# Optimization experiments

Measured on AMD Instinct MI355X. Metric: run time of the kernel, lower is better.

Reference implementation:

```python
import jax, jax.numpy as jnp
import numpy as np

B, S, HID = 2, 2048, 2048
NH, NKV, D = 32, 8, 64
G = NH // NKV  # kv groups


def rotate_half(x):
    x1, x2 = jnp.split(x, 2, axis=-1)
    return jnp.concatenate([-x2, x1], axis=-1)


def setup_inputs() -> dict:
    key = jax.random.key(0)
    ks = jax.random.split(key, 6)
    hidden_states = jax.random.normal(ks[0], (B, S, HID), dtype=jnp.float32)
    # rotary tables [S, D]
    inv_freq = 1.0 / (10000.0 ** (jnp.arange(0, D, 2, dtype=jnp.float32) / D))
    t = jnp.arange(S, dtype=jnp.float32)
    freqs = jnp.einsum('s,d->sd', t, inv_freq)
    emb = jnp.concatenate([freqs, freqs], axis=-1)
    cos, sin = jnp.cos(emb), jnp.sin(emb)
    # additive causal mask [B,1,S,S]
    causal = jnp.triu(jnp.full((S, S), -1e9, dtype=jnp.float32), k=1)
    attention_mask = jnp.broadcast_to(causal, (B, 1, S, S))
    sc = 0.02
    wq = jax.random.normal(ks[1], (HID, 2 * NH * D), dtype=jnp.float32) * sc
    wk = jax.random.normal(ks[2], (HID, NKV * D), dtype=jnp.float32) * sc
    wv = jax.random.normal(ks[3], (HID, NKV * D), dtype=jnp.float32) * sc
    wo = jax.random.normal(ks[4], (HID, HID), dtype=jnp.float32) * sc
    return {"hidden_states": hidden_states, "cos": cos, "sin": sin,
            "attention_mask": attention_mask, "wq": wq, "wk": wk, "wv": wv, "wo": wo}


def reference(hidden_states, cos, sin, attention_mask, wq, wk, wv, wo):
    b, s, _ = hidden_states.shape
    qg = hidden_states @ wq                      # [B,S,2*NH*D]
    q, gate = jnp.split(qg, 2, axis=-1)
    q = q.reshape(b, s, NH, D).transpose(0, 2, 1, 3)        # [B,NH,S,D]
    k = (hidden_states @ wk).reshape(b, s, NKV, D).transpose(0, 2, 1, 3)
    v = (hidden_states @ wv).reshape(b, s, NKV, D).transpose(0, 2, 1, 3)  # computed, unused (as in source)
    # RoPE (cos/sin broadcast over batch and heads)
    c = cos[None, None]; sn = sin[None, None]
    q = q * c + rotate_half(q) * sn
    k = k * c + rotate_half(k) * sn
    # GQA repeat_kv
    k = jnp.repeat(k, G, axis=1)                 # [B,NH,S,D]
    # no 1/sqrt(d) scaling in source
    attn = jnp.einsum('bhqd,bhkd->bhqk', q, k) + attention_mask
    w = jax.nn.softmax(attn.astype(jnp.float32), axis=-1).astype(q.dtype)
    # NOTE: source multiplies weights by key_states (not value_states) — reproduced faithfully
    out = jnp.einsum('bhqk,bhkd->bhqd', w, k)
    out = out.transpose(0, 2, 1, 3).reshape(b, s, HID)
    out = out * jax.nn.sigmoid(gate)
    return out @ wo
```

## Files before the change

### kernel.cpp

```cpp
#include <hip/hip_runtime.h>

typedef float f32x4 __attribute__((ext_vector_type(4)));
typedef short bf16x8 __attribute__((ext_vector_type(8)));

__device__ __forceinline__ float bf2f(unsigned short h) {
  return __uint_as_float(((unsigned int)h) << 16);
}
__device__ __forceinline__ unsigned short f2bf(float f) {
  unsigned int u = __float_as_uint(f);
  unsigned int r = u + 0x7fffu + ((u >> 16) & 1u);
  return (unsigned short)(r >> 16);
}
__device__ __forceinline__ float fast_exp2(float x) {
  return __builtin_amdgcn_exp2f(x);
}

__device__ __forceinline__ void gload_lds16(const void* g, void* l) {
  __builtin_amdgcn_global_load_lds((const __attribute__((address_space(1))) void*)g,
                                   (__attribute__((address_space(3))) void*)l, 16, 0, 0);
}

__global__ void conv_bf16(const float* __restrict__ src, unsigned short* __restrict__ dst, int n4) {
  for (int i = blockIdx.x * blockDim.x + threadIdx.x; i < n4; i += gridDim.x * blockDim.x) {
    float4 v = ((const float4*)src)[i];
    ushort4 o;
    o.x = f2bf(v.x); o.y = f2bf(v.y); o.z = f2bf(v.z); o.w = f2bf(v.w);
    ((ushort4*)dst)[i] = o;
  }
}

__global__ void tconv(const float* __restrict__ src, unsigned short* __restrict__ dst,
                      int C, int dstRowOff, int dstLD) {
  __shared__ float tile[32][33];
  int c0 = blockIdx.x * 32, r0 = blockIdx.y * 32;
  int tx = threadIdx.x, ty = threadIdx.y;
#pragma unroll
  for (int i = 0; i < 4; ++i)
    tile[ty + i * 8][tx] = src[(size_t)(r0 + ty + i * 8) * C + c0 + tx];
  __syncthreads();
#pragma unroll
  for (int i = 0; i < 4; ++i)
    dst[(size_t)(dstRowOff + c0 + ty + i * 8) * dstLD + r0 + tx] = f2bf(tile[tx][ty + i * 8]);
}

template <typename OutT>
__global__ __launch_bounds__(256) void gemm_bt(const unsigned short* __restrict__ A,
                                               const unsigned short* __restrict__ BT,
                                               OutT* __restrict__ C, int M, int N, int K) {
  __shared__ unsigned short As[128 * 64];
  __shared__ unsigned short Bs[128 * 64];
  const int tid = threadIdx.x;
  const int lane = tid & 63;
  const int wid = tid >> 6;
  const int g = lane >> 4, l15 = lane & 15;
  const int wr = wid >> 1, wc = wid & 1;
  const int bm = blockIdx.y, bn = blockIdx.x;
  const unsigned short* Ab = A + (size_t)bm * 128 * K;
  const unsigned short* Bb = BT + (size_t)bn * 128 * K;
  f32x4 acc[4][4] = {};
  int Rj[4], csj[4];
#pragma unroll
  for (int j = 0; j < 4; ++j) {
    int c = j * 256 + tid;
    Rj[j] = c >> 3;
    csj[j] = ((c & 7) ^ (Rj[j] & 7)) * 8;
  }
  for (int k0 = 0; k0 < K; k0 += 64) {
#pragma unroll
    for (int j = 0; j < 4; ++j) {
      gload_lds16(Ab + (size_t)Rj[j] * K + k0 + csj[j], &As[(j * 256 + (wid << 6)) * 8]);
      gload_lds16(Bb + (size_t)Rj[j] * K + k0 + csj[j], &Bs[(j * 256 + (wid << 6)) * 8]);
    }
    __syncthreads();
    bf16x8 af[4][2], bfr[4][2];
#pragma unroll
    for (int i = 0; i < 4; ++i)
#pragma unroll
      for (int kk = 0; kk < 2; ++kk) {
        int rowa = wr * 64 + i * 16 + l15;
        int cha = ((kk * 4 + g) ^ (rowa & 7)) * 8;
        af[i][kk] = *(const bf16x8*)&As[rowa * 64 + cha];
        int rowb = wc * 64 + i * 16 + l15;
        int chb = ((kk * 4 + g) ^ (rowb & 7)) * 8;
        bfr[i][kk] = *(const bf16x8*)&Bs[rowb * 64 + chb];
      }
    __builtin_amdgcn_s_setprio(1);
#pragma unroll
    for (int kk = 0; kk < 2; ++kk)
#pragma unroll
      for (int i = 0; i < 4; ++i)
#pragma unroll
        for (int j = 0; j < 4; ++j)
          acc[i][j] = __builtin_amdgcn_mfma_f32_16x16x32_bf16(af[i][kk], bfr[j][kk], acc[i][j], 0, 0, 0);
    __builtin_amdgcn_s_setprio(0);
    __syncthreads();
  }
  const int rbase = bm * 128 + wr * 64 + ((lane >> 4) << 2);
  const int cbase = bn * 128 + wc * 64 + l15;
#pragma unroll
  for (int i = 0; i < 4; ++i)
#pragma unroll
    for (int j = 0; j < 4; ++j)
#pragma unroll
      for (int r = 0; r < 4; ++r) {
        int row = rbase + i * 16 + r;
        int col = cbase + j * 16;
        if constexpr (sizeof(OutT) == 2)
          C[(size_t)row * N + col] = f2bf(acc[i][j][r]);
        else
          C[(size_t)row * N + col] = acc[i][j][r];
      }
}

__global__ void rope_qk(const unsigned short* __restrict__ qgk, const float* __restrict__ cosT,
                        const float* __restrict__ sinT, unsigned short* __restrict__ qrope,
                        unsigned short* __restrict__ krope) {
  int head = blockIdx.y;
  int tid = threadIdx.x;
  int d = tid & 63;
  int row = blockIdx.x * 4 + (tid >> 6);
  int b = row >> 11, s = row & 2047;
  int base = (head < 32) ? head * 64 : 4096 + (head - 32) * 64;
  size_t off = (size_t)row * 4608 + base;
  float x = bf2f(qgk[off + d]);
  float xp = bf2f(qgk[off + (d ^ 32)]);
  float c = cosT[s * 64 + d], sn = sinT[s * 64 + d];
  float v = x * c + ((d < 32) ? -xp : xp) * sn;
  if (head < 32)
    qrope[((size_t)(b * 32 + head) * 2048 + s) * 64 + d] = f2bf(v * 1.44269504089f);
  else
    krope[((size_t)(b * 8 + (head - 32)) * 2048 + s) * 64 + d] = f2bf(v);
}

__global__ void ktrans(const unsigned short* __restrict__ krope, unsigned short* __restrict__ kT) {
  __shared__ unsigned short tile[64][65];
  int bh = blockIdx.y;
  int s0 = blockIdx.x * 64;
  const unsigned short* src = krope + (size_t)bh * 2048 * 64;
  unsigned short* dst = kT + (size_t)bh * 64 * 2048;
  int tx = threadIdx.x & 63, ty = threadIdx.x >> 6;
#pragma unroll
  for (int i = 0; i < 16; ++i)
    tile[ty + i * 4][tx] = src[(size_t)(s0 + ty + i * 4) * 64 + tx];
  __syncthreads();
#pragma unroll
  for (int i = 0; i < 16; ++i)
    dst[(size_t)(ty + i * 4) * 2048 + s0 + tx] = tile[tx][ty + i * 4];
}

__global__ __launch_bounds__(256) void attn_fused(const unsigned short* __restrict__ qrope,
                                                  const unsigned short* __restrict__ krope,
                                                  const unsigned short* __restrict__ kT,
                                                  const unsigned short* __restrict__ qgk,
                                                  unsigned short* __restrict__ attng) {
  __shared__ unsigned short Ks[2][64 * 64];
  __shared__ unsigned short KTs[2][64 * 64];
  __shared__ unsigned short Ps[128 * 64];
  const int qblk = 15 - blockIdx.y;
  const int bh = blockIdx.x;
  const int b = bh >> 5, h = bh & 31, kh = h >> 2;
  const int q0 = qblk * 128;
  const int tid = threadIdx.x, lane = tid & 63, wid = tid >> 6;
  const int g = lane >> 4, l15 = lane & 15;
  const unsigned short* Qbase = qrope + ((size_t)(b * 32 + h) * 2048 + q0) * 64;
  const unsigned short* Kbase = krope + (size_t)(b * 8 + kh) * 2048 * 64;
  const unsigned short* KTbase = kT + (size_t)(b * 8 + kh) * 64 * 2048;

#pragma unroll
  for (int j = 0; j < 4; ++j) {
    int F = ((j * 4 + wid) << 10) + (lane << 4);
    int R = F >> 7;
    int cs = ((F >> 4) & 7) ^ (R & 7);
    gload_lds16(Qbase + (size_t)R * 64 + cs * 8, &Ps[(j * 4 + wid) << 9]);
  }
  {
#pragma unroll
    for (int j = 0; j < 2; ++j) {
      int F = ((j * 4 + wid) << 10) + (lane << 4);
      int R = F >> 7;
      int cs = ((F >> 4) & 7) ^ (R & 7);
      gload_lds16(Kbase + (size_t)R * 64 + cs * 8, &Ks[0][(j * 4 + wid) << 9]);
      gload_lds16(KTbase + (size_t)R * 2048 + cs * 8, &KTs[0][(j * 4 + wid) << 9]);
    }
  }
  __syncthreads();

  bf16x8 qf[2][2];
#pragma unroll
  for (int i = 0; i < 2; ++i)
#pragma unroll
    for (int ks = 0; ks < 2; ++ks) {
      int row = wid * 32 + i * 16 + l15;
      int ch = (ks * 4 + g) ^ (row & 7);
      qf[i][ks] = *(const bf16x8*)&Ps[row * 64 + ch * 8];
    }
  __syncthreads();

  f32x4 oaccT[2][4] = {};
  float mrow[2] = {-1e30f, -1e30f}, lrow[2] = {0.f, 0.f};

  const int nt = 2 * qblk + 2;
  for (int t = 0; t < nt; ++t) {
    const int cur = t & 1;
    if (t + 1 < nt) {
      const int nb = cur ^ 1;
#pragma unroll
      for (int j = 0; j < 2; ++j) {
        int F = ((j * 4 + wid) << 10) + (lane << 4);
        int R = F >> 7;
        int cs = ((F >> 4) & 7) ^ (R & 7);
        gload_lds16(Kbase + (size_t)((t + 1) * 64 + R) * 64 + cs * 8, &Ks[nb][(j * 4 + wid) << 9]);
        gload_lds16(KTbase + (size_t)R * 2048 + (t + 1) * 64 + cs * 8, &KTs[nb][(j * 4 + wid) << 9]);
      }
    }
    f32x4 st[2][4] = {};
#pragma unroll
    for (int ks = 0; ks < 2; ++ks) {
      bf16x8 kf[4];
#pragma unroll
      for (int nf = 0; nf < 4; ++nf) {
        int row = nf * 16 + l15;
        int ch = (ks * 4 + g) ^ (row & 7);
        kf[nf] = *(const bf16x8*)&Ks[cur][row * 64 + ch * 8];
      }
      __builtin_amdgcn_s_setprio(1);
#pragma unroll
      for (int i = 0; i < 2; ++i)
#pragma unroll
        for (int nf = 0; nf < 4; ++nf)
          st[i][nf] = __builtin_amdgcn_mfma_f32_16x16x32_bf16(kf[nf], qf[i][ks], st[i][nf], 0, 0, 0);
      __builtin_amdgcn_s_setprio(0);
    }
    if (t >= 2 * qblk) {
#pragma unroll
      for (int i = 0; i < 2; ++i) {
        int qabs = q0 + wid * 32 + i * 16 + l15;
#pragma unroll
        for (int nf = 0; nf < 4; ++nf)
#pragma unroll
          for (int r = 0; r < 4; ++r) {
            int kabs = t * 64 + nf * 16 + 4 * g + r;
            if (kabs > qabs) st[i][nf][r] += -1e9f;
          }
      }
    }
#pragma unroll
    for (int i = 0; i < 2; ++i) {
      float pm = st[i][0][0];
#pragma unroll
      for (int nf = 0; nf < 4; ++nf)
#pragma unroll
        for (int r = 0; r < 4; ++r) pm = fmaxf(pm, st[i][nf][r]);
      pm = fmaxf(pm, __shfl_xor(pm, 16, 64));
      pm = fmaxf(pm, __shfl_xor(pm, 32, 64));
      if (!__all(pm <= mrow[i] + 8.f)) {
        float mnew = fmaxf(mrow[i], pm);
        float scale = fast_exp2(mrow[i] - mnew);
        mrow[i] = mnew;
        lrow[i] *= scale;
#pragma unroll
        for (int df = 0; df < 4; ++df)
#pragma unroll
          for (int r = 0; r < 4; ++r) oaccT[i][df][r] *= scale;
      }
      float rs = 0.f;
#pragma unroll
      for (int nf = 0; nf < 4; ++nf)
#pragma unroll
        for (int r = 0; r < 4; ++r) {
          float p = fast_exp2(st[i][nf][r] - mrow[i]);
          st[i][nf][r] = p;
          rs += p;
        }
      rs += __shfl_xor(rs, 16, 64);
      rs += __shfl_xor(rs, 32, 64);
      lrow[i] += rs;
    }
#pragma unroll
    for (int i = 0; i < 2; ++i) {
      int q = wid * 32 + i * 16 + l15;
#pragma unroll
      for (int nf = 0; nf < 4; ++nf) {
        int k0 = nf * 16 + 4 * g;
        int ch = (k0 >> 3) ^ (q & 7);
        ushort4 pk;
        pk.x = f2bf(st[i][nf][0]);
        pk.y = f2bf(st[i][nf][1]);
        pk.z = f2bf(st[i][nf][2]);
        pk.w = f2bf(st[i][nf][3]);
        *(ushort4*)&Ps[q * 64 + ch * 8 + (k0 & 7)] = pk;
      }
    }
#pragma unroll
    for (int ks = 0; ks < 2; ++ks) {
      bf16x8 pf[2], vf[4];
#pragma unroll
      for (int i = 0; i < 2; ++i) {
        int row = wid * 32 + i * 16 + l15;
        int ch = (ks * 4 + g) ^ (row & 7);
        pf[i] = *(const bf16x8*)&Ps[row * 64 + ch * 8];
      }
#pragma unroll
      for (int df = 0; df < 4; ++df) {
        int row = df * 16 + l15;
        int ch = (ks * 4 + g) ^ (row & 7);
        vf[df] = *(const bf16x8*)&KTs[cur][row * 64 + ch * 8];
      }
      __builtin_amdgcn_s_setprio(1);
#pragma unroll
      for (int i = 0; i < 2; ++i)
#pragma unroll
        for (int df = 0; df < 4; ++df)
          oaccT[i][df] = __builtin_amdgcn_mfma_f32_16x16x32_bf16(vf[df], pf[i], oaccT[i][df], 0, 0, 0);
      __builtin_amdgcn_s_setprio(0);
    }
    __syncthreads();
  }
#pragma unroll
  for (int i = 0; i < 2; ++i) {
    float rl = 1.f / lrow[i];
    int qabs = q0 + wid * 32 + i * 16 + l15;
    size_t grow = (size_t)b * 2048 + qabs;
#pragma unroll
    for (int df = 0; df < 4; ++df) {
      int d0 = df * 16 + 4 * g;
      ushort4 gt = *(const ushort4*)&qgk[grow * 4608 + 2048 + h * 64 + d0];
      ushort4 o;
      float gate, gg;
      gate = bf2f(gt.x); gg = 1.f / (1.f + __expf(-gate)); o.x = f2bf(oaccT[i][df][0] * rl * gg);
      gate = bf2f(gt.y); gg = 1.f / (1.f + __expf(-gate)); o.y = f2bf(oaccT[i][df][1] * rl * gg);
      gate = bf2f(gt.z); gg = 1.f / (1.f + __expf(-gate)); o.z = f2bf(oaccT[i][df][2] * rl * gg);
      gate = bf2f(gt.w); gg = 1.f / (1.f + __expf(-gate)); o.w = f2bf(oaccT[i][df][3] * rl * gg);
      *(ushort4*)&attng[grow * 2048 + h * 64 + d0] = o;
    }
  }
}

extern "C" void kernel_launch(void* const* d_in, const int* in_sizes, int n_in,
                              void* d_out, int out_size, void* d_ws, size_t ws_size,
                              hipStream_t stream) {
  const float* hidden = (const float*)d_in[0];
  const float* cosT = (const float*)d_in[1];
  const float* sinT = (const float*)d_in[2];
  const float* wq = (const float*)d_in[4];
  const float* wk = (const float*)d_in[5];
  const float* wo = (const float*)d_in[7];
  char* ws = (char*)d_ws;
  unsigned short* hb16  = (unsigned short*)(ws + 0);
  unsigned short* wcatT = (unsigned short*)(ws + 16777216);
  unsigned short* woT   = (unsigned short*)(ws + 35651584);
  unsigned short* qgk   = (unsigned short*)(ws + 44040192);
  unsigned short* qrope = (unsigned short*)(ws + 81788928);
  unsigned short* krope = (unsigned short*)(ws + 98566144);
  unsigned short* kTb   = (unsigned short*)(ws + 102760448);
  unsigned short* attng = (unsigned short*)(ws + 106954752);

  conv_bf16<<<dim3(2048), dim3(256), 0, stream>>>(hidden, hb16, 2097152);
  tconv<<<dim3(128, 64), dim3(32, 8), 0, stream>>>(wq, wcatT, 4096, 0, 2048);
  tconv<<<dim3(16, 64), dim3(32, 8), 0, stream>>>(wk, wcatT, 512, 4096, 2048);
  tconv<<<dim3(64, 64), dim3(32, 8), 0, stream>>>(wo, woT, 2048, 0, 2048);
  gemm_bt<unsigned short><<<dim3(36, 32), dim3(256), 0, stream>>>(hb16, wcatT, qgk, 4096, 4608, 2048);
  rope_qk<<<dim3(1024, 40), dim3(256), 0, stream>>>(qgk, cosT, sinT, qrope, krope);
  ktrans<<<dim3(32, 16), dim3(256), 0, stream>>>(krope, kTb);
  attn_fused<<<dim3(64, 16), dim3(256), 0, stream>>>(qrope, krope, kTb, qgk, attng);
  gemm_bt<float><<<dim3(16, 32), dim3(256), 0, stream>>>(attng, woT, (float*)d_out, 4096, 2048, 2048);
}
```

Measured before the change: 249.2 us.

## Fuse RoPE, gate split and K transpose into the QKG projection GEMM epilogue

Replaces the generic QGK GEMM plus separate rope_qk and ktrans kernels with one GEMM whose epilogue applies RoPE to Q and K, writes the gate to its own buffer, and writes both K and K-transposed directly. This removes two kernel launches and the round trip of the full qgk intermediate through global memory. In the attention kernel, Q fragments are now loaded directly from global memory, and max3 and packed bf16 conversion instructions replace scalar code. The K-transposed stores from the epilogue are strided and uncoalesced, which may cost some of the saved traffic.

```diff
diff --git a/kernel.cpp b/kernel.cpp
--- a/kernel.cpp
+++ b/kernel.cpp
@@ -13,6 +13,16 @@
 }
 __device__ __forceinline__ float fast_exp2(float x) {
   return __builtin_amdgcn_exp2f(x);
+}
+__device__ __forceinline__ unsigned cvt_pk_bf16(float lo, float hi) {
+  unsigned d;
+  asm("v_cvt_pk_bf16_f32 %0, %1, %2" : "=v"(d) : "v"(lo), "v"(hi));
+  return d;
+}
+__device__ __forceinline__ float max3f(float a, float b, float c) {
+  float d;
+  asm("v_max3_f32 %0, %1, %2, %3" : "=v"(d) : "v"(a), "v"(b), "v"(c));
+  return d;
 }
 
 __device__ __forceinline__ void gload_lds16(const void* g, void* l) {
@@ -112,46 +122,117 @@
       }
 }
 
-__global__ void rope_qk(const unsigned short* __restrict__ qgk, const float* __restrict__ cosT,
-                        const float* __restrict__ sinT, unsigned short* __restrict__ qrope,
-                        unsigned short* __restrict__ krope) {
-  int head = blockIdx.y;
-  int tid = threadIdx.x;
-  int d = tid & 63;
-  int row = blockIdx.x * 4 + (tid >> 6);
-  int b = row >> 11, s = row & 2047;
-  int base = (head < 32) ? head * 64 : 4096 + (head - 32) * 64;
-  size_t off = (size_t)row * 4608 + base;
-  float x = bf2f(qgk[off + d]);
-  float xp = bf2f(qgk[off + (d ^ 32)]);
-  float c = cosT[s * 64 + d], sn = sinT[s * 64 + d];
-  float v = x * c + ((d < 32) ? -xp : xp) * sn;
-  if (head < 32)
-    qrope[((size_t)(b * 32 + head) * 2048 + s) * 64 + d] = f2bf(v * 1.44269504089f);
-  else
-    krope[((size_t)(b * 8 + (head - 32)) * 2048 + s) * 64 + d] = f2bf(v);
-}
-
-__global__ void ktrans(const unsigned short* __restrict__ krope, unsigned short* __restrict__ kT) {
-  __shared__ unsigned short tile[64][65];
-  int bh = blockIdx.y;
-  int s0 = blockIdx.x * 64;
-  const unsigned short* src = krope + (size_t)bh * 2048 * 64;
-  unsigned short* dst = kT + (size_t)bh * 64 * 2048;
-  int tx = threadIdx.x & 63, ty = threadIdx.x >> 6;
-#pragma unroll
-  for (int i = 0; i < 16; ++i)
-    tile[ty + i * 4][tx] = src[(size_t)(s0 + ty + i * 4) * 64 + tx];
-  __syncthreads();
-#pragma unroll
-  for (int i = 0; i < 16; ++i)
-    dst[(size_t)(ty + i * 4) * 2048 + s0 + tx] = tile[tx][ty + i * 4];
+__global__ __launch_bounds__(256) void gemm_qgk(const unsigned short* __restrict__ A,
+                                                const unsigned short* __restrict__ BT,
+                                                const float* __restrict__ cosT,
+                                                const float* __restrict__ sinT,
+                                                unsigned short* __restrict__ qrope,
+                                                unsigned short* __restrict__ gateb,
+                                                unsigned short* __restrict__ krope,
+                                                unsigned short* __restrict__ kT) {
+  const int K = 2048;
+  __shared__ unsigned short As[128 * 64];
+  __shared__ unsigned short Bs[128 * 64];
+  const int tid = threadIdx.x;
+  const int lane = tid & 63;
+  const int wid = tid >> 6;
+  const int g = lane >> 4, l15 = lane & 15;
+  const int wr = wid >> 1, wc = wid & 1;
+  const int bm = blockIdx.y, bn = blockIdx.x;
+  const unsigned short* Ab = A + (size_t)bm * 128 * K;
+  const unsigned short* Bb = BT + (size_t)bn * 128 * K;
+  f32x4 acc[4][4] = {};
+  int Rj[4], csj[4];
+#pragma unroll
+  for (int j = 0; j < 4; ++j) {
+    int c = j * 256 + tid;
+    Rj[j] = c >> 3;
+    csj[j] = ((c & 7) ^ (Rj[j] & 7)) * 8;
+  }
+  for (int k0 = 0; k0 < K; k0 += 64) {
+#pragma unroll
+    for (int j = 0; j < 4; ++j) {
+      gload_lds16(Ab + (size_t)Rj[j] * K + k0 + csj[j], &As[(j * 256 + (wid << 6)) * 8]);
+      gload_lds16(Bb + (size_t)Rj[j] * K + k0 + csj[j], &Bs[(j * 256 + (wid << 6)) * 8]);
+    }
+    __syncthreads();
+    bf16x8 af[4][2], bfr[4][2];
+#pragma unroll
+    for (int i = 0; i < 4; ++i)
+#pragma unroll
+      for (int kk = 0; kk < 2; ++kk) {
+        int rowa = wr * 64 + i * 16 + l15;
+        int cha = ((kk * 4 + g) ^ (rowa & 7)) * 8;
+        af[i][kk] = *(const bf16x8*)&As[rowa * 64 + cha];
+        int rowb = wc * 64 + i * 16 + l15;
+        int chb = ((kk * 4 + g) ^ (rowb & 7)) * 8;
+        bfr[i][kk] = *(const bf16x8*)&Bs[rowb * 64 + chb];
+      }
+    __builtin_amdgcn_s_setprio(1);
+#pragma unroll
+    for (int kk = 0; kk < 2; ++kk)
+#pragma unroll
+      for (int i = 0; i < 4; ++i)
+#pragma unroll
+        for (int j = 0; j < 4; ++j)
+          acc[i][j] = __builtin_amdgcn_mfma_f32_16x16x32_bf16(af[i][kk], bfr[j][kk], acc[i][j], 0, 0, 0);
+    __builtin_amdgcn_s_setprio(0);
+    __syncthreads();
+  }
+  const int rbase = bm * 128 + wr * 64 + ((lane >> 4) << 2);
+  if (bn < 16) {
+    const int h = bn * 2 + wc;
+#pragma unroll
+    for (int i = 0; i < 4; ++i)
+#pragma unroll
+      for (int j = 0; j < 4; ++j)
+#pragma unroll
+        for (int r = 0; r < 4; ++r) {
+          int row = rbase + i * 16 + r;
+          int b = row >> 11, s = row & 2047;
+          int d = j * 16 + l15;
+          float c = cosT[s * 64 + d], sn = sinT[s * 64 + d];
+          float x = acc[i][j][r], xp = acc[i][j ^ 2][r];
+          float v = x * c + (((j & 2) == 0) ? -xp : xp) * sn;
+          qrope[((size_t)(b * 32 + h) * 2048 + s) * 64 + d] = f2bf(v * 1.44269504089f);
+        }
+  } else if (bn < 32) {
+    const int cb = (bn - 16) * 128 + wc * 64;
+#pragma unroll
+    for (int i = 0; i < 4; ++i)
+#pragma unroll
+      for (int j = 0; j < 4; ++j)
+#pragma unroll
+        for (int r = 0; r < 4; ++r) {
+          int row = rbase + i * 16 + r;
+          int b = row >> 11, s = row & 2047;
+          gateb[(size_t)(b * 2048 + s) * 2048 + cb + j * 16 + l15] = f2bf(acc[i][j][r]);
+        }
+  } else {
+    const int kh = (bn - 32) * 2 + wc;
+#pragma unroll
+    for (int i = 0; i < 4; ++i)
+#pragma unroll
+      for (int j = 0; j < 4; ++j)
+#pragma unroll
+        for (int r = 0; r < 4; ++r) {
+          int row = rbase + i * 16 + r;
+          int b = row >> 11, s = row & 2047;
+          int d = j * 16 + l15;
+          float c = cosT[s * 64 + d], sn = sinT[s * 64 + d];
+          float x = acc[i][j][r], xp = acc[i][j ^ 2][r];
+          float v = x * c + (((j & 2) == 0) ? -xp : xp) * sn;
+          unsigned short bv = f2bf(v);
+          krope[((size_t)(b * 8 + kh) * 2048 + s) * 64 + d] = bv;
+          kT[((size_t)(b * 8 + kh) * 64 + d) * 2048 + s] = bv;
+        }
+  }
 }
 
 __global__ __launch_bounds__(256) void attn_fused(const unsigned short* __restrict__ qrope,
                                                   const unsigned short* __restrict__ krope,
                                                   const unsigned short* __restrict__ kT,
-                                                  const unsigned short* __restrict__ qgk,
+                                                  const unsigned short* __restrict__ gateb,
                                                   unsigned short* __restrict__ attng) {
   __shared__ unsigned short Ks[2][64 * 64];
   __shared__ unsigned short KTs[2][64 * 64];
@@ -167,33 +248,19 @@
   const unsigned short* KTbase = kT + (size_t)(b * 8 + kh) * 64 * 2048;
 
 #pragma unroll
-  for (int j = 0; j < 4; ++j) {
+  for (int j = 0; j < 2; ++j) {
     int F = ((j * 4 + wid) << 10) + (lane << 4);
     int R = F >> 7;
     int cs = ((F >> 4) & 7) ^ (R & 7);
-    gload_lds16(Qbase + (size_t)R * 64 + cs * 8, &Ps[(j * 4 + wid) << 9]);
-  }
-  {
-#pragma unroll
-    for (int j = 0; j < 2; ++j) {
-      int F = ((j * 4 + wid) << 10) + (lane << 4);
-      int R = F >> 7;
-      int cs = ((F >> 4) & 7) ^ (R & 7);
-      gload_lds16(Kbase + (size_t)R * 64 + cs * 8, &Ks[0][(j * 4 + wid) << 9]);
-      gload_lds16(KTbase + (size_t)R * 2048 + cs * 8, &KTs[0][(j * 4 + wid) << 9]);
-    }
-  }
-  __syncthreads();
-
+    gload_lds16(Kbase + (size_t)R * 64 + cs * 8, &Ks[0][(j * 4 + wid) << 9]);
+    gload_lds16(KTbase + (size_t)R * 2048 + cs * 8, &KTs[0][(j * 4 + wid) << 9]);
+  }
   bf16x8 qf[2][2];
 #pragma unroll
   for (int i = 0; i < 2; ++i)
 #pragma unroll
-    for (int ks = 0; ks < 2; ++ks) {
-      int row = wid * 32 + i * 16 + l15;
-      int ch = (ks * 4 + g) ^ (row & 7);
-      qf[i][ks] = *(const bf16x8*)&Ps[row * 64 + ch * 8];
-    }
+    for (int ks = 0; ks < 2; ++ks)
+      qf[i][ks] = *(const bf16x8*)(Qbase + (size_t)(wid * 32 + i * 16 + l15) * 64 + ks * 32 + g * 8);
   __syncthreads();
 
   f32x4 oaccT[2][4] = {};
@@ -246,11 +313,12 @@
     }
 #pragma unroll
     for (int i = 0; i < 2; ++i) {
-      float pm = st[i][0][0];
-#pragma unroll
-      for (int nf = 0; nf < 4; ++nf)
-#pragma unroll
-        for (int r = 0; r < 4; ++r) pm = fmaxf(pm, st[i][nf][r]);
+      float a0 = max3f(st[i][0][0], st[i][0][1], st[i][0][2]);
+      float a1 = max3f(st[i][0][3], st[i][1][0], st[i][1][1]);
+      float a2 = max3f(st[i][1][2], st[i][1][3], st[i][2][0]);
+      float a3 = max3f(st[i][2][1], st[i][2][2], st[i][2][3]);
+      float a4 = max3f(st[i][3][0], st[i][3][1], st[i][3][2]);
+      float pm = fmaxf(max3f(a0, a1, a2), max3f(a3, a4, st[i][3][3]));
       pm = fmaxf(pm, __shfl_xor(pm, 16, 64));
       pm = fmaxf(pm, __shfl_xor(pm, 32, 64));
       if (!__all(pm <= mrow[i] + 8.f)) {
@@ -283,12 +351,9 @@
       for (int nf = 0; nf < 4; ++nf) {
         int k0 = nf * 16 + 4 * g;
         int ch = (k0 >> 3) ^ (q & 7);
-        ushort4 pk;
-        pk.x = f2bf(st[i][nf][0]);
-        pk.y = f2bf(st[i][nf][1]);
-        pk.z = f2bf(st[i][nf][2]);
-        pk.w = f2bf(st[i][nf][3]);
-        *(ushort4*)&Ps[q * 64 + ch * 8 + (k0 & 7)] = pk;
+        unsigned w0 = cvt_pk_bf16(st[i][nf][0], st[i][nf][1]);
+        unsigned w1 = cvt_pk_bf16(st[i][nf][2], st[i][nf][3]);
+        *(uint2*)&Ps[q * 64 + ch * 8 + (k0 & 7)] = make_uint2(w0, w1);
       }
     }
 #pragma unroll
@@ -324,14 +389,13 @@
 #pragma unroll
     for (int df = 0; df < 4; ++df) {
       int d0 = df * 16 + 4 * g;
-      ushort4 gt = *(const ushort4*)&qgk[grow * 4608 + 2048 + h * 64 + d0];
-      ushort4 o;
-      float gate, gg;
-      gate = bf2f(gt.x); gg = 1.f / (1.f + __expf(-gate)); o.x = f2bf(oaccT[i][df][0] * rl * gg);
-      gate = bf2f(gt.y); gg = 1.f / (1.f + __expf(-gate)); o.y = f2bf(oaccT[i][df][1] * rl * gg);
-      gate = bf2f(gt.z); gg = 1.f / (1.f + __expf(-gate)); o.z = f2bf(oaccT[i][df][2] * rl * gg);
-      gate = bf2f(gt.w); gg = 1.f / (1.f + __expf(-gate)); o.w = f2bf(oaccT[i][df][3] * rl * gg);
-      *(ushort4*)&attng[grow * 2048 + h * 64 + d0] = o;
+      ushort4 gt = *(const ushort4*)&gateb[grow * 2048 + h * 64 + d0];
+      float o0 = oaccT[i][df][0] * rl * (1.f / (1.f + __expf(-bf2f(gt.x))));
+      float o1 = oaccT[i][df][1] * rl * (1.f / (1.f + __expf(-bf2f(gt.y))));
+      float o2 = oaccT[i][df][2] * rl * (1.f / (1.f + __expf(-bf2f(gt.z))));
+      float o3 = oaccT[i][df][3] * rl * (1.f / (1.f + __expf(-bf2f(gt.w))));
+      *(uint2*)&attng[grow * 2048 + h * 64 + d0] =
+          make_uint2(cvt_pk_bf16(o0, o1), cvt_pk_bf16(o2, o3));
     }
   }
 }
@@ -349,19 +413,18 @@
   unsigned short* hb16  = (unsigned short*)(ws + 0);
   unsigned short* wcatT = (unsigned short*)(ws + 16777216);
   unsigned short* woT   = (unsigned short*)(ws + 35651584);
-  unsigned short* qgk   = (unsigned short*)(ws + 44040192);
-  unsigned short* qrope = (unsigned short*)(ws + 81788928);
-  unsigned short* krope = (unsigned short*)(ws + 98566144);
-  unsigned short* kTb   = (unsigned short*)(ws + 102760448);
-  unsigned short* attng = (unsigned short*)(ws + 106954752);
+  unsigned short* gateb = (unsigned short*)(ws + 44040192);
+  unsigned short* qrope = (unsigned short*)(ws + 60817408);
+  unsigned short* krope = (unsigned short*)(ws + 77594624);
+  unsigned short* kTb   = (unsigned short*)(ws + 81788928);
+  unsigned short* attng = (unsigned short*)(ws + 85983232);
 
   conv_bf16<<<dim3(2048), dim3(256), 0, stream>>>(hidden, hb16, 2097152);
   tconv<<<dim3(128, 64), dim3(32, 8), 0, stream>>>(wq, wcatT, 4096, 0, 2048);
   tconv<<<dim3(16, 64), dim3(32, 8), 0, stream>>>(wk, wcatT, 512, 4096, 2048);
   tconv<<<dim3(64, 64), dim3(32, 8), 0, stream>>>(wo, woT, 2048, 0, 2048);
-  gemm_bt<unsigned short><<<dim3(36, 32), dim3(256), 0, stream>>>(hb16, wcatT, qgk, 4096, 4608, 2048);
-  rope_qk<<<dim3(1024, 40), dim3(256), 0, stream>>>(qgk, cosT, sinT, qrope, krope);
-  ktrans<<<dim3(32, 16), dim3(256), 0, stream>>>(krope, kTb);
-  attn_fused<<<dim3(64, 16), dim3(256), 0, stream>>>(qrope, krope, kTb, qgk, attng);
+  gemm_qgk<<<dim3(36, 32), dim3(256), 0, stream>>>(hb16, wcatT, cosT, sinT,
+                                                   qrope, gateb, krope, kTb);
+  attn_fused<<<dim3(64, 16), dim3(256), 0, stream>>>(qrope, krope, kTb, gateb, attng);
   gemm_bt<float><<<dim3(16, 32), dim3(256), 0, stream>>>(attng, woT, (float*)d_out, 4096, 2048, 2048);
 }
```

Measured after the change: 306.1 us. +22.8%, slower.
